# Performance work log

Hardware: AMD Instinct MI355X
Metric: run time of the kernel (lower is better)

Reference implementation:

```python
import jax, jax.numpy as jnp
import numpy as np

B, T, DIM = 4, 1024, 1024
COND = 1024
HEADS, DH = 16, 64
INNER = HEADS * DH
MLP = 4096
EPS = 1e-5


def setup_inputs() -> dict:
    key = jax.random.key(0)
    ks = jax.random.split(key, 12)
    s = 0.02
    return {
        "x": jax.random.normal(ks[0], (B, T, DIM), jnp.float32),
        "c": jax.random.normal(ks[1], (B, 1, COND), jnp.float32),
        # AdaLN modulation Linear (zero-init in the original; randomized here to exercise all paths)
        "W_mod": jax.random.normal(ks[2], (COND, 6 * DIM), jnp.float32) * s,
        "b_mod": jax.random.normal(ks[3], (6 * DIM,), jnp.float32) * s,
        # attention
        "W_qkv": jax.random.normal(ks[4], (DIM, 3 * INNER), jnp.float32) * s,
        "W_out": jax.random.normal(ks[5], (INNER, DIM), jnp.float32) * s,
        "b_out": jax.random.normal(ks[6], (DIM,), jnp.float32) * s,
        # feed-forward
        "W1": jax.random.normal(ks[7], (DIM, MLP), jnp.float32) * s,
        "b1": jax.random.normal(ks[8], (MLP,), jnp.float32) * s,
        "W2": jax.random.normal(ks[9], (MLP, DIM), jnp.float32) * s,
        "b2": jax.random.normal(ks[10], (DIM,), jnp.float32) * s,
    }


def _layernorm(x):
    # affine-free LayerNorm over last dim
    mu = jnp.mean(x, axis=-1, keepdims=True)
    var = jnp.mean(jnp.square(x - mu), axis=-1, keepdims=True)
    return (x - mu) * jax.lax.rsqrt(var + EPS)


def _modulate(x, shift, scale):
    return x * (1.0 + scale) + shift


def _attention(x, W_qkv, W_out, b_out):
    Bq, Tq, _ = x.shape
    qkv = x @ W_qkv  # [B,T,3*INNER]
    q, k, v = jnp.split(qkv, 3, axis=-1)
    q = q.reshape(Bq, Tq, HEADS, DH)
    k = k.reshape(Bq, Tq, HEADS, DH)
    v = v.reshape(Bq, Tq, HEADS, DH)
    scale = DH ** -0.5
    attn = jnp.einsum("bqhd,bkhd->bhqk", q, k) * scale
    attn = jax.nn.softmax(attn, axis=-1)
    out = jnp.einsum("bhqk,bkhd->bqhd", attn, v).reshape(Bq, Tq, INNER)
    return out @ W_out + b_out


def _ff(x, W1, b1, W2, b2):
    return jax.nn.gelu(x @ W1 + b1, approximate=False) @ W2 + b2


def reference(x, c, W_mod, b_mod, W_qkv, W_out, b_out, W1, b1, W2, b2):
    mod = jax.nn.silu(c) @ W_mod + b_mod  # [B,1,6*DIM]
    sh_msa, sc_msa, g_msa, sh_mlp, sc_mlp, g_mlp = jnp.split(mod, 6, axis=-1)
    x = x + g_msa * _attention(_modulate(_layernorm(x), sh_msa, sc_msa), W_qkv, W_out, b_out)
    x = x + g_mlp * _ff(_modulate(_layernorm(x), sh_mlp, sc_mlp), W1, b1, W2, b2)
    return x
```

## Files before the change

### kernel.cpp

```cpp
#include <hip/hip_runtime.h>
#include <hip/hip_bf16.h>
#include <math.h>

#define BB 4
#define TT 1024
#define DIM 1024
#define HEADS 16
#define DH 64
#define INNER 1024
#define MLP 4096

#define OFF_SH_MSA 0
#define OFF_SC_MSA 1024
#define OFF_G_MSA  2048
#define OFF_SH_MLP 3072
#define OFF_SC_MLP 4096
#define OFF_G_MLP  5120

typedef __attribute__((ext_vector_type(8))) short bf16x8;
typedef __attribute__((ext_vector_type(4))) float fx4;

__device__ __forceinline__ unsigned short f2bf(float f) {
    __hip_bfloat16 h = __float2bfloat16(f);
    return __builtin_bit_cast(unsigned short, h);
}

__device__ __forceinline__ void gload_lds16(const void* g, void* l) {
    __builtin_amdgcn_global_load_lds((const __attribute__((address_space(1))) void*)g,
                                     (__attribute__((address_space(3))) void*)l, 16, 0, 0);
}

__global__ __launch_bounds__(256) void mod_partial(
    const float* __restrict__ c, const float* __restrict__ W_mod,
    float* __restrict__ part)
{
    __shared__ float sc[BB][128];
    int tid = threadIdx.x;
    int ks = blockIdx.y;
    int k0 = ks * 128;
    for (int i = tid; i < BB * 128; i += 256) {
        int bq = i >> 7, kk = i & 127;
        float v = c[bq * 1024 + k0 + kk];
        sc[bq][kk] = v / (1.0f + __expf(-v));
    }
    __syncthreads();
    int n = blockIdx.x * 256 + tid;
    float a0 = 0.f, a1 = 0.f, a2 = 0.f, a3 = 0.f;
    for (int kk = 0; kk < 128; kk++) {
        float w = W_mod[(size_t)(k0 + kk) * 6144 + n];
        a0 += sc[0][kk] * w;
        a1 += sc[1][kk] * w;
        a2 += sc[2][kk] * w;
        a3 += sc[3][kk] * w;
    }
    float* p = part + (size_t)ks * 4 * 6144 + n;
    p[0]        = a0;
    p[6144]     = a1;
    p[2 * 6144] = a2;
    p[3 * 6144] = a3;
}

__global__ __launch_bounds__(256) void mod_reduce(
    const float* __restrict__ part, const float* __restrict__ b_mod,
    float* __restrict__ mod)
{
    int n = blockIdx.x * 256 + threadIdx.x;
    float bb = b_mod[n];
    #pragma unroll
    for (int bq = 0; bq < 4; bq++) {
        float a = bb;
        #pragma unroll
        for (int ks = 0; ks < 8; ks++) a += part[(size_t)(ks * 4 + bq) * 6144 + n];
        mod[bq * 6144 + n] = a;
    }
}

__global__ __launch_bounds__(256) void ln_mod_kernel(
    const float* __restrict__ x, const float* __restrict__ mod,
    int sh_off, int sc_off, unsigned short* __restrict__ out)
{
    int row = blockIdx.x;
    int b = row >> 10;
    const float* xr = x + (size_t)row * DIM;
    float4 v = ((const float4*)xr)[threadIdx.x];

    float s1 = v.x + v.y + v.z + v.w;
    float s2 = v.x * v.x + v.y * v.y + v.z * v.z + v.w * v.w;
    #pragma unroll
    for (int off = 32; off > 0; off >>= 1) {
        s1 += __shfl_down(s1, off, 64);
        s2 += __shfl_down(s2, off, 64);
    }
    __shared__ float red[8];
    int lane = threadIdx.x & 63, w = threadIdx.x >> 6;
    if (lane == 0) { red[w] = s1; red[4 + w] = s2; }
    __syncthreads();
    s1 = red[0] + red[1] + red[2] + red[3];
    s2 = red[4] + red[5] + red[6] + red[7];
    float mu = s1 * (1.0f / DIM);
    float var = s2 * (1.0f / DIM) - mu * mu;
    float rs = rsqrtf(var + 1e-5f);

    int col = threadIdx.x * 4;
    const float* mb = mod + (size_t)b * 6144;
    float4 sc4 = *(const float4*)(mb + sc_off + col);
    float4 sh4 = *(const float4*)(mb + sh_off + col);
    ushort4 o;
    o.x = f2bf((v.x - mu) * rs * (1.0f + sc4.x) + sh4.x);
    o.y = f2bf((v.y - mu) * rs * (1.0f + sc4.y) + sh4.y);
    o.z = f2bf((v.z - mu) * rs * (1.0f + sc4.z) + sh4.z);
    o.w = f2bf((v.w - mu) * rs * (1.0f + sc4.w) + sh4.w);
    ((ushort4*)(out + (size_t)row * DIM))[threadIdx.x] = o;
}

__global__ __launch_bounds__(256) void wcvt_all(
    const float* __restrict__ Wqkv, const float* __restrict__ Wout,
    const float* __restrict__ W1,   const float* __restrict__ W2,
    unsigned short* __restrict__ oQ, unsigned short* __restrict__ oO,
    unsigned short* __restrict__ o1, unsigned short* __restrict__ o2)
{
    __shared__ float tile[32][33];
    int t = blockIdx.x;
    const float* W; unsigned short* O; int K, N, nx;
    if (t < 3072)      {            W = Wqkv; O = oQ; K = 1024; N = 3072; nx = 96;  }
    else if (t < 4096) { t -= 3072; W = Wout; O = oO; K = 1024; N = 1024; nx = 32;  }
    else if (t < 8192) { t -= 4096; W = W1;   O = o1; K = 1024; N = 4096; nx = 128; }
    else               { t -= 8192; W = W2;   O = o2; K = 4096; N = 1024; nx = 32;  }
    int n0 = (t % nx) * 32, k0 = (t / nx) * 32;
    int tx = threadIdx.x & 31, ty = threadIdx.x >> 5;
    #pragma unroll
    for (int i = 0; i < 4; i++)
        tile[ty + i * 8][tx] = W[(size_t)(k0 + ty + i * 8) * N + n0 + tx];
    __syncthreads();
    #pragma unroll
    for (int i = 0; i < 4; i++)
        O[(size_t)(n0 + ty + i * 8) * K + k0 + tx] = f2bf(tile[tx][ty + i * 8]);
}

template<int EPI, int OBF, int NF>
__global__ __launch_bounds__(256) void bgemm(
    const unsigned short* __restrict__ A, const unsigned short* __restrict__ Bt,
    const float* __restrict__ bias, const float* __restrict__ res,
    const float* __restrict__ mod, int gate_off,
    void* __restrict__ Cout, int M, int N, int K)
{
    __shared__ unsigned short Atile[128 * 32];
    __shared__ unsigned short Btile[NF * 32 * 32];
    const int tid = threadIdx.x;
    const int lane = tid & 63, wid = tid >> 6;

    const int gx = gridDim.x;
    const int nwg = gx * gridDim.y;
    const int bid = blockIdx.y * gx + blockIdx.x;
    const int swz = (bid & 7) * (nwg >> 3) + (bid >> 3);
    const int row0 = (swz / gx) * 128;
    const int col0 = (swz % gx) * (NF * 32);

    const int wr = wid >> 1, wc = wid & 1;

    fx4 acc[4][NF];
    const fx4 zero = {0.f, 0.f, 0.f, 0.f};
    #pragma unroll
    for (int m = 0; m < 4; m++)
        #pragma unroll
        for (int n = 0; n < NF; n++) acc[m][n] = zero;

    const int kg = (lane >> 4) * 8;
    const int rl = lane & 15;

    for (int k0 = 0; k0 < K; k0 += 32) {
        #pragma unroll
        for (int i = 0; i < 2; i++) {
            int chunk = wid + i * 4;
            int eo = chunk * 512 + lane * 8;
            int r = eo >> 5, cc = eo & 31;
            gload_lds16(A + (size_t)(row0 + r) * K + k0 + cc, Atile + eo);
        }
        #pragma unroll
        for (int i = 0; i < (NF >> 1); i++) {
            int chunk = wid + i * 4;
            int eo = chunk * 512 + lane * 8;
            int r = eo >> 5, cc = eo & 31;
            gload_lds16(Bt + (size_t)(col0 + r) * K + k0 + cc, Btile + eo);
        }
        __syncthreads();

        bf16x8 af[4], bfr[NF];
        #pragma unroll
        for (int m = 0; m < 4; m++)
            af[m] = *(const bf16x8*)(Atile + (wr * 64 + m * 16 + rl) * 32 + kg);
        #pragma unroll
        for (int n = 0; n < NF; n++)
            bfr[n] = *(const bf16x8*)(Btile + (wc * (NF * 16) + n * 16 + rl) * 32 + kg);
        #pragma unroll
        for (int m = 0; m < 4; m++)
            #pragma unroll
            for (int n = 0; n < NF; n++)
                acc[m][n] = __builtin_amdgcn_mfma_f32_16x16x32_bf16(
                    af[m], bfr[n], acc[m][n], 0, 0, 0);
        __syncthreads();
    }

    const int b = row0 >> 10;
    const int lrow = (lane >> 4) * 4;
    #pragma unroll
    for (int m = 0; m < 4; m++) {
        #pragma unroll
        for (int n = 0; n < NF; n++) {
            int col = col0 + wc * (NF * 16) + n * 16 + rl;
            float bv = 0.f, gate = 0.f;
            if (EPI != 0) bv = bias[col];
            if (EPI == 2) gate = mod[(size_t)b * 6144 + gate_off + col];
            #pragma unroll
            for (int j = 0; j < 4; j++) {
                int row = row0 + wr * 64 + m * 16 + lrow + j;
                float v = acc[m][n][j];
                if (EPI == 1) {
                    float u = v + bv;
                    v = 0.5f * u * (1.0f + erff(u * 0.70710678118654752f));
                } else if (EPI == 2) {
                    v = res[(size_t)row * N + col] + gate * (v + bv);
                }
                if (OBF) ((unsigned short*)Cout)[(size_t)row * N + col] = f2bf(v);
                else     ((float*)Cout)[(size_t)row * N + col] = v;
            }
        }
    }
}

__global__ __launch_bounds__(256) void attn_mfma(
    const unsigned short* __restrict__ qkv, unsigned short* __restrict__ out)
{
    __shared__ unsigned short K_l[64 * 64];
    __shared__ unsigned short VT_l[64 * 64];
    __shared__ unsigned short P_l[4 * 16 * 64];

    const int tid = threadIdx.x;
    const int lane = tid & 63, w = tid >> 6;
    const int rl = lane & 15, lg = lane >> 4;

    const int bid = blockIdx.x;
    const int swz = (bid & 7) * 128 + (bid >> 3);
    const int qi = swz & 15;
    const int bh = swz >> 4;
    const int b = bh >> 4, h = bh & 15;

    const unsigned short* base = qkv + (size_t)b * TT * 3 * INNER + h * DH;

    const int qrow = qi * 64 + w * 16 + rl;
    bf16x8 qf[2];
    qf[0] = *(const bf16x8*)(base + (size_t)qrow * 3 * INNER + lg * 8);
    qf[1] = *(const bf16x8*)(base + (size_t)qrow * 3 * INNER + lg * 8 + 32);

    const fx4 z4 = {0.f, 0.f, 0.f, 0.f};
    fx4 acc_o[4];
    #pragma unroll
    for (int db = 0; db < 4; db++) acc_o[db] = z4;
    float mrow[4] = {-INFINITY, -INFINITY, -INFINITY, -INFINITY};
    float lrow[4] = {0.f, 0.f, 0.f, 0.f};

    unsigned short* Pw = P_l + w * 1024;

    for (int kt = 0; kt < 16; kt++) {
        __syncthreads();
        #pragma unroll
        for (int i = 0; i < 2; i++) {
            int instr = w * 2 + i;
            int row = instr * 8 + (lane >> 3);
            int slog = (lane & 7) ^ (lane >> 3);
            gload_lds16(base + (size_t)(kt * 64 + row) * 3 * INNER + INNER + slog * 8,
                        K_l + instr * 512);
        }
        #pragma unroll
        for (int hh = 0; hh < 2; hh++) {
            int dc = tid & 7;
            int kr = (tid >> 3) + hh * 32;
            const unsigned short* vg =
                base + (size_t)(kt * 64 + kr) * 3 * INNER + 2 * INNER + dc * 8;
            uint4 vv = *(const uint4*)vg;
            unsigned wds[4] = {vv.x, vv.y, vv.z, vv.w};
            #pragma unroll
            for (int j = 0; j < 8; j++) {
                unsigned word = wds[j >> 1];
                unsigned short e = (j & 1) ? (unsigned short)(word >> 16)
                                           : (unsigned short)(word & 0xffff);
                int d = dc * 8 + j;
                int phys = ((kr >> 3) ^ j ^ dc) & 7;
                VT_l[d * 64 + phys * 8 + (kr & 7)] = e;
            }
        }
        __syncthreads();

        fx4 sacc[4];
        #pragma unroll
        for (int kb = 0; kb < 4; kb++) sacc[kb] = z4;
        #pragma unroll
        for (int half = 0; half < 2; half++) {
            #pragma unroll
            for (int kb = 0; kb < 4; kb++) {
                int kr = kb * 16 + rl;
                bf16x8 kf = *(const bf16x8*)(
                    K_l + kr * 64 + (((lg + half * 4) ^ (kr & 7)) & 7) * 8);
                sacc[kb] = __builtin_amdgcn_mfma_f32_16x16x32_bf16(
                    qf[half], kf, sacc[kb], 0, 0, 0);
            }
        }

        #pragma unroll
        for (int kb = 0; kb < 4; kb++) sacc[kb] *= 0.125f;

        float f[4], p[4][4];
        #pragma unroll
        for (int j = 0; j < 4; j++) {
            float t = fmaxf(fmaxf(sacc[0][j], sacc[1][j]),
                            fmaxf(sacc[2][j], sacc[3][j]));
            t = fmaxf(t, __shfl_xor(t, 1));
            t = fmaxf(t, __shfl_xor(t, 2));
            t = fmaxf(t, __shfl_xor(t, 4));
            t = fmaxf(t, __shfl_xor(t, 8));
            float nm = fmaxf(mrow[j], t);
            f[j] = __expf(mrow[j] - nm);
            mrow[j] = nm;
        }
        #pragma unroll
        for (int kb = 0; kb < 4; kb++)
            #pragma unroll
            for (int j = 0; j < 4; j++)
                p[kb][j] = __expf(sacc[kb][j] - mrow[j]);
        #pragma unroll
        for (int j = 0; j < 4; j++) {
            float s = (p[0][j] + p[1][j]) + (p[2][j] + p[3][j]);
            s += __shfl_xor(s, 1);
            s += __shfl_xor(s, 2);
            s += __shfl_xor(s, 4);
            s += __shfl_xor(s, 8);
            lrow[j] = lrow[j] * f[j] + s;
        }
        fx4 fv = {f[0], f[1], f[2], f[3]};
        #pragma unroll
        for (int db = 0; db < 4; db++) acc_o[db] *= fv;

        #pragma unroll
        for (int kb = 0; kb < 4; kb++) {
            #pragma unroll
            for (int j = 0; j < 4; j++) {
                int q16 = lg * 4 + j;
                int phys = ((kb * 2 + (rl >> 3)) ^ (q16 & 7)) & 7;
                Pw[q16 * 64 + phys * 8 + (rl & 7)] = f2bf(p[kb][j]);
            }
        }
        asm volatile("s_waitcnt lgkmcnt(0)" ::: "memory");

        #pragma unroll
        for (int half = 0; half < 2; half++) {
            bf16x8 pf = *(const bf16x8*)(
                Pw + rl * 64 + (((lg + half * 4) ^ (rl & 7)) & 7) * 8);
            #pragma unroll
            for (int db = 0; db < 4; db++) {
                int d = db * 16 + rl;
                bf16x8 vf = *(const bf16x8*)(
                    VT_l + d * 64 +
                    ((((lg + half * 4) ^ (d & 7)) ^ ((d >> 3) & 7)) & 7) * 8);
                acc_o[db] = __builtin_amdgcn_mfma_f32_16x16x32_bf16(
                    pf, vf, acc_o[db], 0, 0, 0);
            }
        }
    }

    float inv[4];
    #pragma unroll
    for (int j = 0; j < 4; j++) inv[j] = 1.0f / lrow[j];
    #pragma unroll
    for (int db = 0; db < 4; db++) {
        #pragma unroll
        for (int j = 0; j < 4; j++) {
            int row = qi * 64 + w * 16 + lg * 4 + j;
            out[(size_t)(b * TT + row) * INNER + h * DH + db * 16 + rl] =
                f2bf(acc_o[db][j] * inv[j]);
        }
    }
}

extern "C" void kernel_launch(void* const* d_in, const int* in_sizes, int n_in,
                              void* d_out, int out_size, void* d_ws, size_t ws_size,
                              hipStream_t stream)
{
    const float* x     = (const float*)d_in[0];
    const float* c     = (const float*)d_in[1];
    const float* W_mod = (const float*)d_in[2];
    const float* b_mod = (const float*)d_in[3];
    const float* W_qkv = (const float*)d_in[4];
    const float* W_out = (const float*)d_in[5];
    const float* b_out = (const float*)d_in[6];
    const float* W1    = (const float*)d_in[7];
    const float* b1    = (const float*)d_in[8];
    const float* W2    = (const float*)d_in[9];
    const float* b2    = (const float*)d_in[10];
    float* out = (float*)d_out;

    const int M = BB * TT;

    char* ws = (char*)d_ws;
    float* mod      = (float*)ws;
    float* mod_part = (float*)(ws + 131072);
    float* x1       = (float*)(ws + 1048576);
    unsigned short* bb = (unsigned short*)(ws + 1048576 + (size_t)M * DIM * 4);
    unsigned short* Wqkv_t = bb;  bb += (size_t)3 * INNER * DIM;
    unsigned short* Wout_t = bb;  bb += (size_t)DIM * INNER;
    unsigned short* W1_t   = bb;  bb += (size_t)MLP * DIM;
    unsigned short* W2_t   = bb;  bb += (size_t)DIM * MLP;
    unsigned short* xm     = bb;  bb += (size_t)M * DIM;
    unsigned short* qkvb   = bb;  bb += (size_t)M * 3 * INNER;
    unsigned short* attnb  = bb;  bb += (size_t)M * INNER;
    unsigned short* xm2    = bb;  bb += (size_t)M * DIM;
    unsigned short* hbuf   = bb;  bb += (size_t)M * MLP;

    wcvt_all<<<12288, 256, 0, stream>>>(W_qkv, W_out, W1, W2,
                                        Wqkv_t, Wout_t, W1_t, W2_t);

    mod_partial<<<dim3(24, 8), 256, 0, stream>>>(c, W_mod, mod_part);
    mod_reduce<<<24, 256, 0, stream>>>(mod_part, b_mod, mod);
    ln_mod_kernel<<<M, 256, 0, stream>>>(x, mod, OFF_SH_MSA, OFF_SC_MSA, xm);
    bgemm<0, 1, 4><<<dim3(3 * INNER / 128, M / 128), 256, 0, stream>>>(
        xm, Wqkv_t, nullptr, nullptr, nullptr, 0, qkvb, M, 3 * INNER, DIM);
    attn_mfma<<<BB * HEADS * (TT / 64), 256, 0, stream>>>(qkvb, attnb);
    bgemm<2, 0, 2><<<dim3(DIM / 64, M / 128), 256, 0, stream>>>(
        attnb, Wout_t, b_out, x, mod, OFF_G_MSA, x1, M, DIM, INNER);
    ln_mod_kernel<<<M, 256, 0, stream>>>(x1, mod, OFF_SH_MLP, OFF_SC_MLP, xm2);
    bgemm<1, 1, 4><<<dim3(MLP / 128, M / 128), 256, 0, stream>>>(
        xm2, W1_t, b1, nullptr, nullptr, 0, hbuf, M, MLP, DIM);
    bgemm<2, 0, 2><<<dim3(DIM / 64, M / 128), 256, 0, stream>>>(
        hbuf, W2_t, b2, x1, mod, OFF_G_MLP, out, M, DIM, MLP);
}
```

Baseline: 436.9 us.

## Replace GEMMs with 256x256 multi-stage pipelined kernel and split-K FF2

Replaces the 128-row GEMM with a 256x256-tile, 512-thread kernel that uses a 4-deep LDS ring buffer with direct global-to-LDS loads, swizzled LDS layout, and explicit vmcnt waits so loads overlap MFMA work. The second feed-forward GEMM is split along K into two slices written as fp32 partials, and a new elementwise kernel sums them and applies bias, gate and residual. This raises data reuse per tile and hides memory latency, but uses much more LDS and registers per block and launches few blocks for the narrow GEMMs, which the split-K only partly offsets. It also adds an extra fp32 pass over the output for the split-K reduction.

```diff
diff --git a/kernel.cpp b/kernel.cpp
--- a/kernel.cpp
+++ b/kernel.cpp
@@ -137,83 +137,103 @@
         O[(size_t)(n0 + ty + i * 8) * K + k0 + tx] = f2bf(tile[tx][ty + i * 8]);
 }
 
-template<int EPI, int OBF, int NF>
-__global__ __launch_bounds__(256) void bgemm(
-    const unsigned short* __restrict__ A, const unsigned short* __restrict__ Bt,
+template<int EPI, int OBF>
+__global__ __launch_bounds__(512, 2) void bgemm256(
+    const unsigned short* __restrict__ A0, const unsigned short* __restrict__ Bt0,
     const float* __restrict__ bias, const float* __restrict__ res,
     const float* __restrict__ mod, int gate_off,
-    void* __restrict__ Cout, int M, int N, int K)
-{
-    __shared__ unsigned short Atile[128 * 32];
-    __shared__ unsigned short Btile[NF * 32 * 32];
+    void* __restrict__ Cout, int M, int N, int Klen, int lda, int ldb,
+    int kz, int zout)
+{
+    __shared__ unsigned short As[4][8192];
+    __shared__ unsigned short Bs[4][8192];
+
     const int tid = threadIdx.x;
     const int lane = tid & 63, wid = tid >> 6;
+    const int rl = lane & 15, lg = lane >> 4;
+    const int rl4 = rl & 3;
+    const int wr = wid >> 2, wc = wid & 3;
 
     const int gx = gridDim.x;
     const int nwg = gx * gridDim.y;
     const int bid = blockIdx.y * gx + blockIdx.x;
     const int swz = (bid & 7) * (nwg >> 3) + (bid >> 3);
-    const int row0 = (swz / gx) * 128;
-    const int col0 = (swz % gx) * (NF * 32);
-
-    const int wr = wid >> 1, wc = wid & 1;
-
-    fx4 acc[4][NF];
+    const int row0 = (swz / gx) * 256;
+    const int col0 = (swz % gx) * 256;
+
+    const unsigned short* A  = A0  + (size_t)blockIdx.z * kz;
+    const unsigned short* Bt = Bt0 + (size_t)blockIdx.z * kz;
+
+    const int rA = tid >> 2;
+    const int pA = tid & 3;
+    const int sA = (pA ^ (rA & 3)) * 8;
+    const unsigned short* a0p = A  + (size_t)(row0 + rA) * lda + sA;
+    const unsigned short* a1p = A  + (size_t)(row0 + 128 + rA) * lda + sA;
+    const unsigned short* b0p = Bt + (size_t)(col0 + rA) * ldb + sA;
+    const unsigned short* b1p = Bt + (size_t)(col0 + 128 + rA) * ldb + sA;
+
+    fx4 acc[8][4];
     const fx4 zero = {0.f, 0.f, 0.f, 0.f};
     #pragma unroll
-    for (int m = 0; m < 4; m++)
-        #pragma unroll
-        for (int n = 0; n < NF; n++) acc[m][n] = zero;
-
-    const int kg = (lane >> 4) * 8;
-    const int rl = lane & 15;
-
-    for (int k0 = 0; k0 < K; k0 += 32) {
-        #pragma unroll
-        for (int i = 0; i < 2; i++) {
-            int chunk = wid + i * 4;
-            int eo = chunk * 512 + lane * 8;
-            int r = eo >> 5, cc = eo & 31;
-            gload_lds16(A + (size_t)(row0 + r) * K + k0 + cc, Atile + eo);
-        }
-        #pragma unroll
-        for (int i = 0; i < (NF >> 1); i++) {
-            int chunk = wid + i * 4;
-            int eo = chunk * 512 + lane * 8;
-            int r = eo >> 5, cc = eo & 31;
-            gload_lds16(Bt + (size_t)(col0 + r) * K + k0 + cc, Btile + eo);
-        }
-        __syncthreads();
-
-        bf16x8 af[4], bfr[NF];
-        #pragma unroll
-        for (int m = 0; m < 4; m++)
-            af[m] = *(const bf16x8*)(Atile + (wr * 64 + m * 16 + rl) * 32 + kg);
-        #pragma unroll
-        for (int n = 0; n < NF; n++)
-            bfr[n] = *(const bf16x8*)(Btile + (wc * (NF * 16) + n * 16 + rl) * 32 + kg);
-        #pragma unroll
-        for (int m = 0; m < 4; m++)
-            #pragma unroll
-            for (int n = 0; n < NF; n++)
+    for (int m = 0; m < 8; m++)
+        #pragma unroll
+        for (int n = 0; n < 4; n++) acc[m][n] = zero;
+
+    const int NT = Klen >> 5;
+
+#define STAGE256(q, kt) do {                                   \
+        int koff = (kt) << 5;                                  \
+        gload_lds16(a0p + koff, As[q] + tid * 8);              \
+        gload_lds16(a1p + koff, As[q] + 4096 + tid * 8);       \
+        gload_lds16(b0p + koff, Bs[q] + tid * 8);              \
+        gload_lds16(b1p + koff, Bs[q] + 4096 + tid * 8);       \
+    } while (0)
+
+    STAGE256(0, 0);
+    STAGE256(1, 1);
+    STAGE256(2, 2);
+
+    const int ro = (lg ^ rl4) * 8;
+    for (int t = 0; t < NT; ++t) {
+        if (t < NT - 2)       asm volatile("s_waitcnt vmcnt(8)" ::: "memory");
+        else if (t == NT - 2) asm volatile("s_waitcnt vmcnt(4)" ::: "memory");
+        else                  asm volatile("s_waitcnt vmcnt(0)" ::: "memory");
+        __builtin_amdgcn_s_barrier();
+        if (t + 3 < NT) STAGE256((t + 3) & 3, t + 3);
+
+        const int q = t & 3;
+        bf16x8 bfr[4], af[8];
+        #pragma unroll
+        for (int n = 0; n < 4; n++)
+            bfr[n] = *(const bf16x8*)(Bs[q] + (wc * 64 + n * 16 + rl) * 32 + ro);
+        #pragma unroll
+        for (int m = 0; m < 8; m++)
+            af[m] = *(const bf16x8*)(As[q] + (wr * 128 + m * 16 + rl) * 32 + ro);
+        __builtin_amdgcn_s_setprio(1);
+        #pragma unroll
+        for (int m = 0; m < 8; m++)
+            #pragma unroll
+            for (int n = 0; n < 4; n++)
                 acc[m][n] = __builtin_amdgcn_mfma_f32_16x16x32_bf16(
                     af[m], bfr[n], acc[m][n], 0, 0, 0);
-        __syncthreads();
-    }
+        __builtin_amdgcn_s_setprio(0);
+    }
+#undef STAGE256
 
     const int b = row0 >> 10;
-    const int lrow = (lane >> 4) * 4;
-    #pragma unroll
-    for (int m = 0; m < 4; m++) {
-        #pragma unroll
-        for (int n = 0; n < NF; n++) {
-            int col = col0 + wc * (NF * 16) + n * 16 + rl;
+    unsigned short* outb = (unsigned short*)Cout + (size_t)blockIdx.z * zout;
+    float* outf = (float*)Cout + (size_t)blockIdx.z * zout;
+    #pragma unroll
+    for (int m = 0; m < 8; m++) {
+        #pragma unroll
+        for (int n = 0; n < 4; n++) {
+            int col = col0 + wc * 64 + n * 16 + rl;
             float bv = 0.f, gate = 0.f;
-            if (EPI != 0) bv = bias[col];
+            if (EPI == 1 || EPI == 2) bv = bias[col];
             if (EPI == 2) gate = mod[(size_t)b * 6144 + gate_off + col];
             #pragma unroll
             for (int j = 0; j < 4; j++) {
-                int row = row0 + wr * 64 + m * 16 + lrow + j;
+                int row = row0 + wr * 128 + m * 16 + lg * 4 + j;
                 float v = acc[m][n][j];
                 if (EPI == 1) {
                     float u = v + bv;
@@ -221,11 +241,32 @@
                 } else if (EPI == 2) {
                     v = res[(size_t)row * N + col] + gate * (v + bv);
                 }
-                if (OBF) ((unsigned short*)Cout)[(size_t)row * N + col] = f2bf(v);
-                else     ((float*)Cout)[(size_t)row * N + col] = v;
+                if (OBF) outb[(size_t)row * N + col] = f2bf(v);
+                else     outf[(size_t)row * N + col] = v;
             }
         }
     }
+}
+
+__global__ __launch_bounds__(256) void ff2_fin(
+    const float* __restrict__ part, const float* __restrict__ x1,
+    const float* __restrict__ mod, const float* __restrict__ b2,
+    float* __restrict__ out)
+{
+    int i = (blockIdx.x * 256 + threadIdx.x) * 4;
+    int col = i & 1023;
+    int b = i >> 20;
+    float4 p0 = *(const float4*)(part + i);
+    float4 p1 = *(const float4*)(part + 4194304 + i);
+    float4 r  = *(const float4*)(x1 + i);
+    float4 g  = *(const float4*)(mod + (size_t)b * 6144 + OFF_G_MLP + col);
+    float4 bb = *(const float4*)(b2 + col);
+    float4 o;
+    o.x = r.x + g.x * (bb.x + p0.x + p1.x);
+    o.y = r.y + g.y * (bb.y + p0.y + p1.y);
+    o.z = r.z + g.z * (bb.z + p0.z + p1.z);
+    o.w = r.w + g.w * (bb.w + p0.w + p1.w);
+    *(float4*)(out + i) = o;
 }
 
 __global__ __launch_bounds__(256) void attn_mfma(
@@ -414,6 +455,7 @@
     unsigned short* attnb  = bb;  bb += (size_t)M * INNER;
     unsigned short* xm2    = bb;  bb += (size_t)M * DIM;
     unsigned short* hbuf   = bb;  bb += (size_t)M * MLP;
+    float* ff2part = (float*)xm;
 
     wcvt_all<<<12288, 256, 0, stream>>>(W_qkv, W_out, W1, W2,
                                         Wqkv_t, Wout_t, W1_t, W2_t);
@@ -421,14 +463,19 @@
     mod_partial<<<dim3(24, 8), 256, 0, stream>>>(c, W_mod, mod_part);
     mod_reduce<<<24, 256, 0, stream>>>(mod_part, b_mod, mod);
     ln_mod_kernel<<<M, 256, 0, stream>>>(x, mod, OFF_SH_MSA, OFF_SC_MSA, xm);
-    bgemm<0, 1, 4><<<dim3(3 * INNER / 128, M / 128), 256, 0, stream>>>(
-        xm, Wqkv_t, nullptr, nullptr, nullptr, 0, qkvb, M, 3 * INNER, DIM);
+    bgemm256<0, 1><<<dim3(12, 16), 512, 0, stream>>>(
+        xm, Wqkv_t, nullptr, nullptr, nullptr, 0, qkvb,
+        M, 3 * INNER, DIM, DIM, DIM, 0, 0);
     attn_mfma<<<BB * HEADS * (TT / 64), 256, 0, stream>>>(qkvb, attnb);
-    bgemm<2, 0, 2><<<dim3(DIM / 64, M / 128), 256, 0, stream>>>(
-        attnb, Wout_t, b_out, x, mod, OFF_G_MSA, x1, M, DIM, INNER);
+    bgemm256<2, 0><<<dim3(4, 16), 512, 0, stream>>>(
+        attnb, Wout_t, b_out, x, mod, OFF_G_MSA, x1,
+        M, DIM, INNER, INNER, INNER, 0, 0);
     ln_mod_kernel<<<M, 256, 0, stream>>>(x1, mod, OFF_SH_MLP, OFF_SC_MLP, xm2);
-    bgemm<1, 1, 4><<<dim3(MLP / 128, M / 128), 256, 0, stream>>>(
-        xm2, W1_t, b1, nullptr, nullptr, 0, hbuf, M, MLP, DIM);
-    bgemm<2, 0, 2><<<dim3(DIM / 64, M / 128), 256, 0, stream>>>(
-        hbuf, W2_t, b2, x1, mod, OFF_G_MLP, out, M, DIM, MLP);
-}
+    bgemm256<1, 1><<<dim3(16, 16), 512, 0, stream>>>(
+        xm2, W1_t, b1, nullptr, nullptr, 0, hbuf,
+        M, MLP, DIM, DIM, DIM, 0, 0);
+    bgemm256<3, 0><<<dim3(4, 16, 2), 512, 0, stream>>>(
+        hbuf, W2_t, nullptr, nullptr, nullptr, 0, ff2part,
+        M, DIM, MLP / 2, MLP, MLP, MLP / 2, M * DIM);
+    ff2_fin<<<M * DIM / 1024, 256, 0, stream>>>(ff2part, x1, mod, b2, out);
+}
```

Result: slower. 479.6 us (+9.8%).
